# Performance work log

Measured on AMD Instinct MI355X. Metric: run time of the kernel, lower is better.

## Reference

```python
import jax, jax.numpy as jnp
import numpy as np

EPS = 1e-4
IN_DIM, D1, D2 = 30, 20, 15


def _orthogonal(key, rows, cols):
    # mimic nn.init.orthogonal_ for a (rows, cols) matrix with rows < cols
    a = jax.random.normal(key, (cols, rows), dtype=jnp.float32)
    q, _ = jnp.linalg.qr(a)  # (cols, rows) with orthonormal columns
    return q.T  # (rows, cols), rows orthonormal


def setup_inputs() -> dict:
    key = jax.random.key(0)
    kx, k1, k2 = jax.random.split(key, 3)
    X = jax.random.normal(kx, (65536, IN_DIM, IN_DIM), dtype=jnp.float32)
    W1 = _orthogonal(k1, D1, IN_DIM)
    W2 = _orthogonal(k2, D2, D1)
    return {"X": X, "W1": W1, "W2": W2}


def _bimap(X, W):
    # W @ X @ W^T, symmetrized, + eps*I  -> (b, out, out)
    Y = jnp.einsum('oi,bij,pj->bop', W, X, W)
    Y = (Y + jnp.swapaxes(Y, -1, -2)) * 0.5
    return Y + EPS * jnp.eye(W.shape[0], dtype=Y.dtype)


def _reeig(X):
    w, v = jnp.linalg.eigh(X)
    w = jnp.maximum(w, EPS)
    return jnp.einsum('bik,bk,bjk->bij', v, w, v)


def _logeig(X):
    w, v = jnp.linalg.eigh(X)
    w = jnp.log(jnp.maximum(w, EPS))
    return jnp.einsum('bik,bk,bjk->bij', v, w, v)


def reference(X, W1, W2):
    X = _reeig(_bimap(X, W1))            # (b, 20, 20)
    X = _logeig(_reeig(_bimap(X, W2)))   # (b, 15, 15)
    iu0, iu1 = jnp.triu_indices(D2)      # row-major upper-tri, matches torch.triu_indices
    return X[:, iu0, iu1]                # (b, 120)
```

## Files before the change

kernel.cpp:

```cpp
#include <hip/hip_runtime.h>

#define EPSV 1e-4f

__device__ __forceinline__ float bperm(int addr4, float v) {
  return __int_as_float(__builtin_amdgcn_ds_bpermute(addr4, __float_as_int(v)));
}

template<int N>
__device__ __forceinline__ float selN(const float (&a)[N], int idx) {
  float r = a[0];
#pragma unroll
  for (int k = 1; k < N; ++k) r = (idx == k) ? a[k] : r;
  return r;
}

template<int N>
__device__ void jacobi_eig(float (&a)[N], float (&v)[N], int l, int base4,
                           bool laneValid, float tolsq, int maxSweeps)
{
  constexpr int NH = N / 2;
  const int partner = N - 1 - l;
  const int pslot = (l < NH) ? l : partner;
  const int qslot = N - 1 - pslot;
  const int p4 = base4 + 4 * pslot;
  const int q4 = base4 + 4 * qslot;
  const int pr4 = base4 + 4 * partner;
  const int srcl = (l == 0) ? 0 : ((l == 1) ? (N - 1) : (l - 1));
  const int src4 = base4 + 4 * srcl;
  const bool isP = (l < NH);

  float dval = selN<N>(a, l);
  int sweep = 0;
  while (true) {
    float offAcc = 0.0f;
    for (int r = 0; r < N - 1; ++r) {
      float anti = selN<N>(a, partner);
      float app = bperm(p4, dval);
      float aqq = bperm(q4, dval);
      float apq = bperm(p4, anti);

      float absq = fabsf(apq);
      bool ok = absq > 1e-28f;
      float apqs = ok ? apq : 1.0f;
      float theta = 0.5f * (aqq - app) / apqs;
      float tt = 1.0f / (fabsf(theta) + sqrtf(theta * theta + 1.0f));
      tt = (theta < 0.0f) ? -tt : tt;
      tt = ok ? tt : 0.0f;
      float c = 1.0f / sqrtf(tt * tt + 1.0f);
      float s = tt * c;
      offAcc += laneValid ? apq * apq : 0.0f;

      float seff = isP ? -s : s;
#pragma unroll
      for (int k = 0; k < N; ++k) {
        float pc = bperm(pr4, a[k]);
        a[k] = c * a[k] + seff * pc;
      }
#pragma unroll
      for (int i = 0; i < NH; ++i) {
        float ci = bperm(base4 + 4 * i, c);
        float si = bperm(base4 + 4 * i, s);
        float x = a[i], y = a[N - 1 - i];
        a[i]         = ci * x - si * y;
        a[N - 1 - i] = si * x + ci * y;
        float xv = v[i], yv = v[N - 1 - i];
        v[i]         = ci * xv - si * yv;
        v[N - 1 - i] = si * xv + ci * yv;
      }
      float dnew = isP ? (app - tt * apq) : (aqq + tt * apq);

      float tmp[N];
#pragma unroll
      for (int k = 0; k < N; ++k) tmp[k] = bperm(src4, a[k]);
      a[0] = tmp[0];
      a[1] = tmp[N - 1];
#pragma unroll
      for (int k = 2; k < N; ++k) a[k] = tmp[k - 1];
      float xl = v[N - 1];
#pragma unroll
      for (int k = N - 1; k >= 2; --k) v[k] = v[k - 1];
      v[1] = xl;
      dval = bperm(src4, dnew);
    }
    ++sweep;
#pragma unroll
    for (int m = 1; m < 64; m <<= 1) offAcc += __shfl_xor(offAcc, m);
    if (sweep >= maxSweeps || offAcc < tolsq) break;
  }
}

__global__ __launch_bounds__(256, 3)
void spdnet_kernel(const float* __restrict__ X, const float* __restrict__ W1g,
                   const float* __restrict__ W2g, float* __restrict__ out,
                   int nBatch)
{
  __shared__ __align__(16) float sW1[20 * 32];
  __shared__ __align__(16) float sW2[15 * 20];
  __shared__ __align__(16) float sS[4 * 3 * 964];

  const int tid = threadIdx.x;
  const int wave = tid >> 6;
  const int lane = tid & 63;
  const int grp = lane / 20;
  const int l = lane - grp * 20;
  const int g3 = (grp < 3) ? grp : 2;
  const bool activeG = (grp < 3);
  const int wstart = blockIdx.x * 12 + wave * 3;
  const int bm = wstart + g3;
  const bool valid = activeG && (bm < nBatch);
  const int base4 = g3 * 80;
  float* sSw = sS + wave * (3 * 964);
  float* Sm = sSw + g3 * 964;

  for (int i = tid; i < 600; i += 256) sW1[(i / 30) * 32 + (i % 30)] = W1g[i];
  for (int i = tid; i < 300; i += 256) sW2[i] = W2g[i];

  int nm = nBatch - wstart; nm = nm < 0 ? 0 : (nm > 3 ? 3 : nm);
  const float* Xg = X + (size_t)wstart * 900;
  for (int idx = lane; idx < nm * 900; idx += 64) {
    int m = idx / 900;
    int rem = idx - m * 900;
    int r = rem / 30;
    int kk = rem - r * 30;
    sSw[m * 964 + r * 32 + kk] = Xg[idx];
  }
  __syncthreads();

  for (int t0 = lane; t0 < 2700; t0 += 64) {
    int m = t0 / 900;
    int rem = t0 - m * 900;
    int i = rem / 30;
    int j = rem - i * 30;
    if (i < j && m < nm) {
      float* Sp = sSw + m * 964;
      float x = Sp[i * 32 + j], y = Sp[j * 32 + i];
      float h = 0.5f * (x + y);
      Sp[i * 32 + j] = h;
      Sp[j * 32 + i] = h;
    }
  }
  __syncthreads();

  float w1r[30];
  {
    const float2* wr = (const float2*)(W1g + l * 30);
#pragma unroll
    for (int k2 = 0; k2 < 15; ++k2) {
      float2 q = wr[k2];
      w1r[2 * k2] = q.x; w1r[2 * k2 + 1] = q.y;
    }
  }
  float tcol[30];
#pragma unroll
  for (int r = 0; r < 30; ++r) {
    const float* row = Sm + r * 32;
    const float4* row4 = (const float4*)row;
    float acc = 0.0f;
#pragma unroll
    for (int k4 = 0; k4 < 7; ++k4) {
      float4 q = row4[k4];
      acc += q.x * w1r[4 * k4] + q.y * w1r[4 * k4 + 1] +
             q.z * w1r[4 * k4 + 2] + q.w * w1r[4 * k4 + 3];
    }
    acc += row[28] * w1r[28] + row[29] * w1r[29];
    tcol[r] = acc;
  }
  float a[20], v[20];
#pragma unroll
  for (int i = 0; i < 20; ++i) {
    const float* wrow = sW1 + i * 32;
    const float4* w4 = (const float4*)wrow;
    float acc = 0.0f;
#pragma unroll
    for (int k4 = 0; k4 < 7; ++k4) {
      float4 q = w4[k4];
      acc += q.x * tcol[4 * k4] + q.y * tcol[4 * k4 + 1] +
             q.z * tcol[4 * k4 + 2] + q.w * tcol[4 * k4 + 3];
    }
    acc += wrow[28] * tcol[28] + wrow[29] * tcol[29];
    a[i] = acc + ((i == l) ? EPSV : 0.0f);
    v[i] = (i == l) ? 1.0f : 0.0f;
  }

  jacobi_eig<20>(a, v, l, base4, valid, 2.0e-9f, 12);

  float lam1 = selN<20>(a, l);
  float gs = sqrtf(fmaxf(lam1, EPSV));

  float* Vl = Sm;
  if (activeG) {
#pragma unroll
    for (int k = 0; k < 20; ++k) Vl[l * 21 + k] = v[k];
  }
  __syncthreads();
  float vcol[20];
#pragma unroll
  for (int r = 0; r < 20; ++r) vcol[r] = Vl[r * 21 + l];
  float* Ut = Sm + 448;
  float b[15];
#pragma unroll
  for (int i = 0; i < 15; ++i) {
    const float4* w2r = (const float4*)(sW2 + i * 20);
    float acc = 0.0f;
#pragma unroll
    for (int r4 = 0; r4 < 5; ++r4) {
      float4 q = w2r[r4];
      acc += q.x * vcol[4 * r4] + q.y * vcol[4 * r4 + 1] +
             q.z * vcol[4 * r4 + 2] + q.w * vcol[4 * r4 + 3];
    }
    b[i] = acc;
  }
  if (activeG) {
#pragma unroll
    for (int i = 0; i < 15; ++i) Ut[i * 20 + l] = gs * b[i];
  }
  __syncthreads();

  const int l2 = l & 15;
  float myrow[20];
  {
    const float4* mr = (const float4*)(Ut + ((l2 < 15) ? l2 : 0) * 20);
    float msk = (l2 < 15) ? 1.0f : 0.0f;
#pragma unroll
    for (int r4 = 0; r4 < 5; ++r4) {
      float4 q = mr[r4];
      myrow[4 * r4]     = q.x * msk; myrow[4 * r4 + 1] = q.y * msk;
      myrow[4 * r4 + 2] = q.z * msk; myrow[4 * r4 + 3] = q.w * msk;
    }
  }
  float a2[16], v2[16];
  a2[15] = 0.0f;
#pragma unroll
  for (int r = 0; r < 15; ++r) {
    const float4* ur = (const float4*)(Ut + r * 20);
    float acc = 0.0f;
#pragma unroll
    for (int r4 = 0; r4 < 5; ++r4) {
      float4 q = ur[r4];
      acc += q.x * myrow[4 * r4] + q.y * myrow[4 * r4 + 1] +
             q.z * myrow[4 * r4 + 2] + q.w * myrow[4 * r4 + 3];
    }
    a2[r] = acc + ((r == l2) ? EPSV : 0.0f);
  }
#pragma unroll
  for (int k = 0; k < 16; ++k) v2[k] = (k == l2) ? 1.0f : 0.0f;

  jacobi_eig<16>(a2, v2, l2, base4, valid && (l < 16), 3.0e-10f, 12);

  float lam2 = selN<16>(a2, l2);
  float h = logf(fmaxf(lam2, EPSV));

  __syncthreads();
  float* Wl = Sm;
  float* hl = Sm + 768;
  if (activeG && l < 16) {
#pragma unroll
    for (int k = 0; k < 16; ++k) Wl[l2 * 20 + k] = v2[k];
    hl[l2] = h;
  }
  __syncthreads();

  if (valid && l < 15) {
    float wj[15], hw[15];
#pragma unroll
    for (int k = 0; k < 15; ++k) wj[k] = Wl[l * 20 + k];
#pragma unroll
    for (int k = 0; k < 15; ++k) hw[k] = hl[k] * wj[k];
    float* og = out + (size_t)bm * 120;
#pragma unroll
    for (int i = 0; i < 15; ++i) {
      const float* wr = Wl + i * 20;
      float acc = 0.0f;
#pragma unroll
      for (int k = 0; k < 15; ++k) acc += hw[k] * wr[k];
      if (i <= l) og[15 * i - (i * (i - 1)) / 2 + (l - i)] = acc;
    }
  }
}

extern "C" void kernel_launch(void* const* d_in, const int* in_sizes, int n_in,
                              void* d_out, int out_size, void* d_ws, size_t ws_size,
                              hipStream_t stream) {
  const float* X  = (const float*)d_in[0];
  const float* W1 = (const float*)d_in[1];
  const float* W2 = (const float*)d_in[2];
  float* out = (float*)d_out;
  int nBatch = in_sizes[0] / 900;
  int nBlocks = (nBatch + 11) / 12;
  spdnet_kernel<<<nBlocks, 256, 0, stream>>>(X, W1, W2, out, nBatch);
}
```

Before: 4.407 ms.

## Stream X directly from global, shrink LDS, use wave-local fences and rsq

Each lane now reads its whole input matrix straight from global memory as float4 and builds the W X column product in registers. Symmetrization moves after the bilinear map via an LDS transpose, and the shared staging of X and the weights is removed. LDS shrinks, launch bounds rise to allow more waves, block barriers become compiler-only fences within the wave, and the Jacobi rotation recomputes c and s from a broadcast tangent using rsq. The risks are uncoalesced per-lane global loads of 900 floats, heavy register pressure under the tighter bound, and reliance on wave-synchronous LDS ordering with no hardware barrier.

```diff
diff --git a/kernel.cpp b/kernel.cpp
--- a/kernel.cpp
+++ b/kernel.cpp
@@ -5,6 +5,8 @@
 __device__ __forceinline__ float bperm(int addr4, float v) {
   return __int_as_float(__builtin_amdgcn_ds_bpermute(addr4, __float_as_int(v)));
 }
+
+__device__ __forceinline__ void wave_fence() { asm volatile("" ::: "memory"); }
 
 template<int N>
 __device__ __forceinline__ float selN(const float (&a)[N], int idx) {
@@ -46,7 +48,7 @@
       float tt = 1.0f / (fabsf(theta) + sqrtf(theta * theta + 1.0f));
       tt = (theta < 0.0f) ? -tt : tt;
       tt = ok ? tt : 0.0f;
-      float c = 1.0f / sqrtf(tt * tt + 1.0f);
+      float c = __builtin_amdgcn_rsqf(tt * tt + 1.0f);
       float s = tt * c;
       offAcc += laneValid ? apq * apq : 0.0f;
 
@@ -58,8 +60,9 @@
       }
 #pragma unroll
       for (int i = 0; i < NH; ++i) {
-        float ci = bperm(base4 + 4 * i, c);
-        float si = bperm(base4 + 4 * i, s);
+        float ti = bperm(base4 + 4 * i, tt);
+        float ci = __builtin_amdgcn_rsqf(ti * ti + 1.0f);
+        float si = ti * ci;
         float x = a[i], y = a[N - 1 - i];
         a[i]         = ci * x - si * y;
         a[N - 1 - i] = si * x + ci * y;
@@ -89,14 +92,12 @@
   }
 }
 
-__global__ __launch_bounds__(256, 3)
+__global__ __launch_bounds__(256, 5)
 void spdnet_kernel(const float* __restrict__ X, const float* __restrict__ W1g,
                    const float* __restrict__ W2g, float* __restrict__ out,
                    int nBatch)
 {
-  __shared__ __align__(16) float sW1[20 * 32];
-  __shared__ __align__(16) float sW2[15 * 20];
-  __shared__ __align__(16) float sS[4 * 3 * 964];
+  __shared__ __align__(16) float sS[12 * 420];
 
   const int tid = threadIdx.x;
   const int wave = tid >> 6;
@@ -109,37 +110,7 @@
   const int bm = wstart + g3;
   const bool valid = activeG && (bm < nBatch);
   const int base4 = g3 * 80;
-  float* sSw = sS + wave * (3 * 964);
-  float* Sm = sSw + g3 * 964;
-
-  for (int i = tid; i < 600; i += 256) sW1[(i / 30) * 32 + (i % 30)] = W1g[i];
-  for (int i = tid; i < 300; i += 256) sW2[i] = W2g[i];
-
-  int nm = nBatch - wstart; nm = nm < 0 ? 0 : (nm > 3 ? 3 : nm);
-  const float* Xg = X + (size_t)wstart * 900;
-  for (int idx = lane; idx < nm * 900; idx += 64) {
-    int m = idx / 900;
-    int rem = idx - m * 900;
-    int r = rem / 30;
-    int kk = rem - r * 30;
-    sSw[m * 964 + r * 32 + kk] = Xg[idx];
-  }
-  __syncthreads();
-
-  for (int t0 = lane; t0 < 2700; t0 += 64) {
-    int m = t0 / 900;
-    int rem = t0 - m * 900;
-    int i = rem / 30;
-    int j = rem - i * 30;
-    if (i < j && m < nm) {
-      float* Sp = sSw + m * 964;
-      float x = Sp[i * 32 + j], y = Sp[j * 32 + i];
-      float h = 0.5f * (x + y);
-      Sp[i * 32 + j] = h;
-      Sp[j * 32 + i] = h;
-    }
-  }
-  __syncthreads();
+  float* Sm = sS + (wave * 3 + g3) * 420;
 
   float w1r[30];
   {
@@ -150,35 +121,46 @@
       w1r[2 * k2] = q.x; w1r[2 * k2 + 1] = q.y;
     }
   }
+
+  const int bmc = (bm < nBatch) ? bm : (nBatch - 1);
+  const float4* Xm = (const float4*)(X + (size_t)bmc * 900);
   float tcol[30];
 #pragma unroll
-  for (int r = 0; r < 30; ++r) {
-    const float* row = Sm + r * 32;
-    const float4* row4 = (const float4*)row;
-    float acc = 0.0f;
-#pragma unroll
-    for (int k4 = 0; k4 < 7; ++k4) {
-      float4 q = row4[k4];
-      acc += q.x * w1r[4 * k4] + q.y * w1r[4 * k4 + 1] +
-             q.z * w1r[4 * k4 + 2] + q.w * w1r[4 * k4 + 3];
-    }
-    acc += row[28] * w1r[28] + row[29] * w1r[29];
-    tcol[r] = acc;
-  }
+  for (int r = 0; r < 30; ++r) tcol[r] = 0.0f;
+#pragma unroll
+  for (int q = 0; q < 225; ++q) {
+    float4 x4 = Xm[q];
+    tcol[(4 * q + 0) / 30] += x4.x * w1r[(4 * q + 0) % 30];
+    tcol[(4 * q + 1) / 30] += x4.y * w1r[(4 * q + 1) % 30];
+    tcol[(4 * q + 2) / 30] += x4.z * w1r[(4 * q + 2) % 30];
+    tcol[(4 * q + 3) / 30] += x4.w * w1r[(4 * q + 3) % 30];
+  }
+
+  float z[20];
+#pragma unroll
+  for (int i = 0; i < 20; ++i) z[i] = 0.0f;
+  {
+    const float4* W14 = (const float4*)W1g;
+#pragma unroll
+    for (int q = 0; q < 150; ++q) {
+      float4 w4 = W14[q];
+      z[(4 * q + 0) / 30] += w4.x * tcol[(4 * q + 0) % 30];
+      z[(4 * q + 1) / 30] += w4.y * tcol[(4 * q + 1) % 30];
+      z[(4 * q + 2) / 30] += w4.z * tcol[(4 * q + 2) % 30];
+      z[(4 * q + 3) / 30] += w4.w * tcol[(4 * q + 3) % 30];
+    }
+  }
+
+  if (activeG) {
+#pragma unroll
+    for (int k = 0; k < 20; ++k) Sm[k * 21 + l] = z[k];
+  }
+  wave_fence();
   float a[20], v[20];
 #pragma unroll
   for (int i = 0; i < 20; ++i) {
-    const float* wrow = sW1 + i * 32;
-    const float4* w4 = (const float4*)wrow;
-    float acc = 0.0f;
-#pragma unroll
-    for (int k4 = 0; k4 < 7; ++k4) {
-      float4 q = w4[k4];
-      acc += q.x * tcol[4 * k4] + q.y * tcol[4 * k4 + 1] +
-             q.z * tcol[4 * k4 + 2] + q.w * tcol[4 * k4 + 3];
-    }
-    acc += wrow[28] * tcol[28] + wrow[29] * tcol[29];
-    a[i] = acc + ((i == l) ? EPSV : 0.0f);
+    float zt = Sm[l * 21 + i];
+    a[i] = 0.5f * (z[i] + zt) + ((i == l) ? EPSV : 0.0f);
     v[i] = (i == l) ? 1.0f : 0.0f;
   }
 
@@ -187,34 +169,37 @@
   float lam1 = selN<20>(a, l);
   float gs = sqrtf(fmaxf(lam1, EPSV));
 
-  float* Vl = Sm;
   if (activeG) {
 #pragma unroll
-    for (int k = 0; k < 20; ++k) Vl[l * 21 + k] = v[k];
-  }
-  __syncthreads();
+    for (int k = 0; k < 20; ++k) Sm[l * 21 + k] = v[k];
+  }
+  wave_fence();
   float vcol[20];
 #pragma unroll
-  for (int r = 0; r < 20; ++r) vcol[r] = Vl[r * 21 + l];
-  float* Ut = Sm + 448;
+  for (int r = 0; r < 20; ++r) vcol[r] = Sm[r * 21 + l];
+
   float b[15];
 #pragma unroll
-  for (int i = 0; i < 15; ++i) {
-    const float4* w2r = (const float4*)(sW2 + i * 20);
-    float acc = 0.0f;
-#pragma unroll
-    for (int r4 = 0; r4 < 5; ++r4) {
-      float4 q = w2r[r4];
-      acc += q.x * vcol[4 * r4] + q.y * vcol[4 * r4 + 1] +
-             q.z * vcol[4 * r4 + 2] + q.w * vcol[4 * r4 + 3];
-    }
-    b[i] = acc;
-  }
+  for (int i = 0; i < 15; ++i) b[i] = 0.0f;
+  {
+    const float4* W24 = (const float4*)W2g;
+#pragma unroll
+    for (int q = 0; q < 75; ++q) {
+      float4 w4 = W24[q];
+      b[(4 * q + 0) / 20] += w4.x * vcol[(4 * q + 0) % 20];
+      b[(4 * q + 1) / 20] += w4.y * vcol[(4 * q + 1) % 20];
+      b[(4 * q + 2) / 20] += w4.z * vcol[(4 * q + 2) % 20];
+      b[(4 * q + 3) / 20] += w4.w * vcol[(4 * q + 3) % 20];
+    }
+  }
+
+  wave_fence();
+  float* Ut = Sm;
   if (activeG) {
 #pragma unroll
     for (int i = 0; i < 15; ++i) Ut[i * 20 + l] = gs * b[i];
   }
-  __syncthreads();
+  wave_fence();
 
   const int l2 = l & 15;
   float myrow[20];
@@ -250,15 +235,15 @@
   float lam2 = selN<16>(a2, l2);
   float h = logf(fmaxf(lam2, EPSV));
 
-  __syncthreads();
+  wave_fence();
   float* Wl = Sm;
-  float* hl = Sm + 768;
+  float* hl = Sm + 400;
   if (activeG && l < 16) {
 #pragma unroll
     for (int k = 0; k < 16; ++k) Wl[l2 * 20 + k] = v2[k];
     hl[l2] = h;
   }
-  __syncthreads();
+  wave_fence();
 
   if (valid && l < 15) {
     float wj[15], hw[15];
```

Result: slower. 4.840 ms (+9.8%).
